# Kernel tuning notes

Hardware: AMD Instinct MI355X
Metric: run time of the kernel (lower is better)

## Reference

```python
import jax, jax.numpy as jnp
import numpy as np

B, N = 2, 6
H, W = 64, 64            # BEV grid
FH, FW = 32, 88          # camera feature map
DIM, FEAT_DIM = 128, 128
HEADS, DH = 4, 32
QW1, QW2 = 8, 8          # query window
KW1, KW2 = 4, 11         # key/val window
IMG_H, IMG_W = 224, 480
EPS = 1e-5


def _ln(t, g, b):
    m = t.mean(-1, keepdims=True)
    v = ((t - m) ** 2).mean(-1, keepdims=True)
    return (t - m) / jnp.sqrt(v + EPS) * g + b


def _bn_relu_conv(t, g, b, Wc):
    # eval-mode BatchNorm2d (running_mean=0, running_var=1) -> ReLU -> 1x1 conv
    y = jax.nn.relu(t / jnp.sqrt(1.0 + EPS) * g[:, None, None] + b[:, None, None])
    return jnp.einsum('oc,nchw->nohw', Wc, y)


def _normalize(t, axis):
    n = jnp.sqrt(jnp.sum(t * t, axis=axis, keepdims=True))
    return t / jnp.maximum(n, 1e-12)


def _win(t, w1, w2):
    # (..., X*w1, Y*w2, d) -> (..., X, Y, w1, w2, d)
    s = t.shape
    t = t.reshape(*s[:-3], s[-3] // w1, w1, s[-2] // w2, w2, s[-1])
    return jnp.swapaxes(t, -4, -3)


def _unwin(t):
    # (..., X, Y, w1, w2, d) -> (..., X*w1, Y*w2, d)
    s = t.shape
    return jnp.swapaxes(t, -4, -3).reshape(*s[:-5], s[-5] * s[-3], s[-4] * s[-2], s[-1])


def _gridwin(t, w1, w2):
    bb, nn, Ht, Wt, d = t.shape
    t = t.reshape(bb, nn, w1, Ht // w1, w2, Wt // w2, d)
    return t.transpose(0, 1, 3, 5, 2, 4, 6)  # (b, n, X, Y, w1, w2, d)


def _cross_win_attn(qw, kw, vw, ln_g, ln_b, Wqkv, bqkv, Wp, bp, skip):
    b, n, X, Y, w1, w2, d = qw.shape
    f1, f2 = kw.shape[4], kw.shape[5]
    L = X * Y
    q = qw.transpose(0, 2, 3, 1, 4, 5, 6).reshape(b, L, n * w1 * w2, d)
    k = kw.transpose(0, 2, 3, 1, 4, 5, 6).reshape(b, L, n * f1 * f2, d)
    v = vw.transpose(0, 2, 3, 1, 4, 5, 6).reshape(b, L, n * f1 * f2, d)
    q = _ln(q, ln_g[0], ln_b[0]) @ Wqkv[0] + bqkv[0]
    k = _ln(k, ln_g[1], ln_b[1]) @ Wqkv[1] + bqkv[1]
    v = _ln(v, ln_g[2], ln_b[2]) @ Wqkv[2] + bqkv[2]
    split = lambda t: t.reshape(*t.shape[:-1], HEADS, DH)  # head-major channel split
    q, k, v = split(q), split(k), split(v)
    att = jax.nn.softmax(DH ** -0.5 * jnp.einsum('blqhd,blkhd->bhlqk', q, k), axis=-1)
    o = jnp.einsum('bhlqk,blkhd->blqhd', att, v).reshape(b, L, n * w1 * w2, HEADS * DH)
    o = o @ Wp + bp
    o = o.reshape(b, X, Y, n, w1, w2, d).mean(3)  # mean over cameras
    return o + skip


def _forward(x, grid, feature, I_inv, E_inv,
             bn_fl_g, bn_fl_b, W_fl, bn_fp_g, bn_fp_b, W_fp,
             W_bev, b_bev, W_img, W_cam,
             attn_ln_g, attn_ln_b, attn_Wqkv, attn_bqkv, attn_Wp, attn_bp,
             pn_g, pn_b, Wma, bma, Wmb, bmb, post_g, post_b):
    b, n = feature.shape[:2]
    # image plane (buffer)
    xs = jnp.linspace(0.0, 1.0, FW) * IMG_W
    ys = jnp.linspace(0.0, 1.0, FH) * IMG_H
    gx, gy = jnp.meshgrid(xs, ys)  # (FH, FW) each
    plane = jnp.stack([gx, gy, jnp.ones_like(gx)], 0).reshape(3, FH * FW)
    # camera embedding from translation column of E_inv
    c = E_inv[..., -1]                                   # (b, n, 4)
    c_embed = jnp.einsum('oc,bnc->bno', W_cam, c)        # (b, n, dim)
    # unprojected rays
    cam = jnp.einsum('bnij,jk->bnik', I_inv, plane)      # (b, n, 3, HW)
    cam = jnp.concatenate([cam, jnp.ones_like(cam[:, :, :1])], 2)
    d = jnp.einsum('bnij,bnjk->bnik', E_inv, cam)        # (b, n, 4, HW)
    d_img = d.reshape(b, n, 4, FH, FW)
    d_embed = jnp.einsum('oc,bnchw->bnohw', W_img, d_img)
    img_embed = _normalize(d_embed - c_embed[..., None, None], axis=2)
    # BEV positional embedding
    w_embed = jnp.einsum('oc,chw->ohw', W_bev, grid[:2]) + b_bev[:, None, None]
    bev_embed = _normalize(w_embed[None, None] - c_embed[..., None, None], axis=2)  # (b,n,dim,H,W)
    feat = feature.reshape(b * n, FEAT_DIM, FH, FW)
    key_im = img_embed + _bn_relu_conv(feat, bn_fp_g, bn_fp_b, W_fp).reshape(b, n, DIM, FH, FW)
    val_im = _bn_relu_conv(feat, bn_fl_g, bn_fl_b, W_fl).reshape(b, n, DIM, FH, FW)
    query = bev_embed + x[:, None]                       # (b, n, dim, H, W)
    # channel-last
    q_im = query.transpose(0, 1, 3, 4, 2)
    k_im = key_im.transpose(0, 1, 3, 4, 2)
    v_im = val_im.transpose(0, 1, 3, 4, 2)
    x_im = x.transpose(0, 2, 3, 1)
    # stage 1: local windows
    qw = _win(q_im, QW1, QW2)
    kw = _win(k_im, KW1, KW2)
    vw = _win(v_im, KW1, KW2)
    o1 = _cross_win_attn(qw, kw, vw, attn_ln_g[0], attn_ln_b[0], attn_Wqkv[0],
                         attn_bqkv[0], attn_Wp[0], attn_bp[0], _win(x_im, QW1, QW2))
    q1 = _unwin(o1)                                      # (b, H, W, d)
    q1 = q1 + jax.nn.gelu(_ln(q1, pn_g[0], pn_b[0]) @ Wma[0] + bma[0], approximate=False) @ Wmb[0] + bmb[0]
    # stage 2: grid (swapped) windows
    qg = jnp.broadcast_to(q1[:, None], (b, n) + q1.shape[1:])
    o2 = _cross_win_attn(_win(qg, QW1, QW2), _gridwin(k_im, KW1, KW2), _gridwin(v_im, KW1, KW2),
                         attn_ln_g[1], attn_ln_b[1], attn_Wqkv[1], attn_bqkv[1],
                         attn_Wp[1], attn_bp[1], _win(q1, QW1, QW2))
    q2 = _unwin(o2)
    q2 = q2 + jax.nn.gelu(_ln(q2, pn_g[1], pn_b[1]) @ Wma[1] + bma[1], approximate=False) @ Wmb[1] + bmb[1]
    out = _ln(q2, post_g, post_b)
    return out.transpose(0, 3, 1, 2)                     # (b, dim, H, W)


def setup_inputs() -> dict:
    key = jax.random.key(0)
    ks = jax.random.split(key, 16)
    rn = lambda i, shape, sc=0.02: jax.random.normal(ks[i], shape, dtype=jnp.float32) * sc
    return {
        'index': 0,
        'x': jax.random.normal(ks[0], (B, DIM, H, W), dtype=jnp.float32),
        'grid': jax.random.normal(ks[1], (2, H, W), dtype=jnp.float32),
        'feature': jax.random.normal(ks[2], (B, N, FEAT_DIM, FH, FW), dtype=jnp.float32),
        'I_inv': jax.random.normal(ks[3], (B, N, 3, 3), dtype=jnp.float32),
        'E_inv': jax.random.normal(ks[4], (B, N, 4, 4), dtype=jnp.float32),
        'bn_fl_g': jnp.ones((FEAT_DIM,), jnp.float32), 'bn_fl_b': jnp.zeros((FEAT_DIM,), jnp.float32),
        'W_fl': rn(5, (DIM, FEAT_DIM)),
        'bn_fp_g': jnp.ones((FEAT_DIM,), jnp.float32), 'bn_fp_b': jnp.zeros((FEAT_DIM,), jnp.float32),
        'W_fp': rn(6, (DIM, FEAT_DIM)),
        'W_bev': rn(7, (DIM, 2)), 'b_bev': jnp.zeros((DIM,), jnp.float32),
        'W_img': rn(8, (DIM, 4)), 'W_cam': rn(9, (DIM, 4)),
        'attn_ln_g': jnp.ones((2, 3, DIM), jnp.float32), 'attn_ln_b': jnp.zeros((2, 3, DIM), jnp.float32),
        'attn_Wqkv': rn(10, (2, 3, DIM, HEADS * DH)), 'attn_bqkv': jnp.zeros((2, 3, HEADS * DH), jnp.float32),
        'attn_Wp': rn(11, (2, HEADS * DH, DIM)), 'attn_bp': jnp.zeros((2, DIM), jnp.float32),
        'pn_g': jnp.ones((2, DIM), jnp.float32), 'pn_b': jnp.zeros((2, DIM), jnp.float32),
        'Wma': rn(12, (2, DIM, 2 * DIM)), 'bma': jnp.zeros((2, 2 * DIM), jnp.float32),
        'Wmb': rn(13, (2, 2 * DIM, DIM)), 'bmb': jnp.zeros((2, DIM), jnp.float32),
        'post_g': jnp.ones((DIM,), jnp.float32), 'post_b': jnp.zeros((DIM,), jnp.float32),
    }


def reference(index, x, grid, feature, I_inv, E_inv,
              bn_fl_g, bn_fl_b, W_fl, bn_fp_g, bn_fp_b, W_fp,
              W_bev, b_bev, W_img, W_cam,
              attn_ln_g, attn_ln_b, attn_Wqkv, attn_bqkv, attn_Wp, attn_bp,
              pn_g, pn_b, Wma, bma, Wmb, bmb, post_g, post_b):
    del index  # grid for this index is passed directly
    return _forward(x, grid, feature, I_inv, E_inv,
                    bn_fl_g, bn_fl_b, W_fl, bn_fp_g, bn_fp_b, W_fp,
                    W_bev, b_bev, W_img, W_cam,
                    attn_ln_g, attn_ln_b, attn_Wqkv, attn_bqkv, attn_Wp, attn_bp,
                    pn_g, pn_b, Wma, bma, Wmb, bmb, post_g, post_b)
```

## Files before the change

kernel.cpp:

```cpp
#include <hip/hip_runtime.h>
#include <math.h>


typedef __attribute__((ext_vector_type(8))) short short8;
typedef __attribute__((ext_vector_type(4))) float f32x4;

__device__ __forceinline__ unsigned short f2bf(float f){
  union { float f; unsigned u; } v; v.f = f;
  unsigned r = v.u + 0x7FFF + ((v.u >> 16) & 1);
  return (unsigned short)(r >> 16);
}
__device__ __forceinline__ float bf2f(unsigned short h){
  union { unsigned u; float f; } v; v.u = ((unsigned)h) << 16; return v.f;
}
__device__ __forceinline__ void store_bf16x8(unsigned short* p, const float* v){
  union { short8 s8; unsigned short u[8]; } u;
  #pragma unroll
  for (int i=0;i<8;i++) u.u[i] = f2bf(v[i]);
  *(short8*)p = u.s8;
}

__device__ __forceinline__ float gelu_erf(float x){
  float z = x * 0.70710678118654752f;
  float a = fabsf(z);
// ... 151 lines not shown
      float sq = 0.f;
      #pragma unroll 8
      for (int k=0;k<64;k++){
        int c = half*64 + k;
        float4 w = sWI4[c];
        float de = w.x*d0 + w.y*d1 + w.z*d2 + w.w*d3 - sCE[c];
        sA[r*KP_ + c] = f2bf(de);
        sq = fmaf(de, de, sq);
      }
      sq += __shfl_xor(sq, 1);
      if (half == 0) sRn[r] = 1.0f / fmaxf(sqrtf(sq), 1e-12f);
    }
    {
      const float* Wsrc = qkv + m1*16384;
      const float* gvv = lg + m1*128;
      for (int idx = tid; idx < 8192; idx += 256){
        int n = idx & 127, k2 = (idx >> 7) << 1;
        float v0 = Wsrc[(size_t)k2*128 + n]     * gvv[k2];
        float v1 = Wsrc[(size_t)(k2+1)*128 + n] * gvv[k2+1];
        *(unsigned*)&sW[n*KP_ + k2] = (unsigned)f2bf(v0) | ((unsigned)f2bf(v1) << 16);
      }
    }
    __syncthreads();
    #pragma unroll
    for (int mt=0; mt<8; mt++){
      #pragma unroll
      for (int nt=0; nt<2; nt++){
        int col = n0 + nt*16 + lane15;
        #pragma unroll
        for (int r4=0; r4<4; r4++){
          int row = mt*16 + quad*4 + r4;
          float v = acc[mt][nt][r4];
          if (!which) v += bf2f(sA[row*KP_ + col]) * sRn[row];
          sA[row*KP_ + col] = f2bf(v);
        }
      }
    }
    __syncthreads();
    {
      int r = tid >> 1, part = tid & 1;
      float s=0.f, s2=0.f;
      #pragma unroll 8
      for (int k=0;k<64;k++){
        float v = bf2f(sA[r*KP_ + part*64 + k]);
        s += v; s2 = fmaf(v,v,s2);
      }
      s += __shfl_xor(s, 1); s2 += __shfl_xor(s2, 1);
      if (part == 0){
        float mean = s*(1.f/128.f);
        sMean[r] = mean;
        sRstd[r] = rsqrtf(fmaxf(s2*(1.f/128.f) - mean*mean, 0.f) + 1e-5f);
      }
    }
    __syncthreads();
    for (int i = tid; i < 2048; i += 256){
      int row = i >> 4, seg = i & 15;
      float mean = sMean[row], rstd = sRstd[row];
      union { short8 s; unsigned short u[8]; } t;
      t.s = *(const short8*)&sA[row*KP_ + seg*8];
      float v[8];
      #pragma unroll
      for (int k=0;k<8;k++) v[k] = (bf2f(t.u[k]) - mean)*rstd;
      store_bf16x8(&sA[row*KP_ + seg*8], v);
    }
    __syncthreads();
    #pragma unroll
    for (int mt=0; mt<8; mt++){ acc[mt][0]=(f32x4)0.f; acc[mt][1]=(f32x4)0.f; }
    #pragma unroll
    for (int kk=0; kk<4; kk++){
      short8 af[8], bf2v[2];
      #pragma unroll
      for (int mt=0; mt<8; mt++) af[mt] = *(const short8*)(aptr + mt*16*KP_ + kk*32);
      bf2v[0] = *(const short8*)(bptr + kk*32);
      bf2v[1] = *(const short8*)(bptr + 16*KP_ + kk*32);
      #pragma unroll
      for (int mt=0; mt<8; mt++){
        acc[mt][0] = __builtin_amdgcn_mfma_f32_16x16x32_bf16(af[mt], bf2v[0], acc[mt][0], 0,0,0);
        acc[mt][1] = __builtin_amdgcn_mfma_f32_16x16x32_bf16(af[mt], bf2v[1], acc[mt][1], 0,0,0);
      }
    }
    __syncthreads();
    #pragma unroll
    for (int mt=0; mt<8; mt++){
      #pragma unroll
      for (int nt=0; nt<2; nt++){
        int col = n0 + nt*16 + lane15;
        float bsv = sB1[col];
        #pragma unroll
        for (int r4=0; r4<4; r4++){
          int row = mt*16 + quad*4 + r4;
          sW[row*KP_ + col] = f2bf(acc[mt][nt][r4] + bsv);
        }
      }
    }
    __syncthreads();
    for (int i = tid; i < 2048; i += 256){
      int row = i >> 4, seg = i & 15;
      size_t orow = remap_kv(base + row, 1);
      *(short8*)(Oa + orow*128 + seg*8) = *(const short8*)&sW[row*KP_ + seg*8];
    }
    __syncthreads();
    {
      const float* Wsrc = qkv + m2*16384;
      const float* gvv = lg + m2*128;
      for (int idx = tid; idx < 8192; idx += 256){
        int n = idx & 127, k2 = (idx >> 7) << 1;
        float v0 = Wsrc[(size_t)k2*128 + n]     * gvv[k2];
        float v1 = Wsrc[(size_t)(k2+1)*128 + n] * gvv[k2+1];
        *(unsigned*)&sW[n*KP_ + k2] = (unsigned)f2bf(v0) | ((unsigned)f2bf(v1) << 16);
      }
    }
    __syncthreads();
    #pragma unroll
    for (int mt=0; mt<8; mt++){ acc[mt][0]=(f32x4)0.f; acc[mt][1]=(f32x4)0.f; }
    #pragma unroll
    for (int kk=0; kk<4; kk++){
      short8 af[8], bf2v[2];
      #pragma unroll
      for (int mt=0; mt<8; mt++) af[mt] = *(const short8*)(aptr + mt*16*KP_ + kk*32);
      bf2v[0] = *(const short8*)(bptr + kk*32);
      bf2v[1] = *(const short8*)(bptr + 16*KP_ + kk*32);
      #pragma unroll
      for (int mt=0; mt<8; mt++){
        acc[mt][0] = __builtin_amdgcn_mfma_f32_16x16x32_bf16(af[mt], bf2v[0], acc[mt][0], 0,0,0);
        acc[mt][1] = __builtin_amdgcn_mfma_f32_16x16x32_bf16(af[mt], bf2v[1], acc[mt][1], 0,0,0);
      }
    }
    __syncthreads();
    #pragma unroll
    for (int mt=0; mt<8; mt++){
      #pragma unroll
      for (int nt=0; nt<2; nt++){
        int col = n0 + nt*16 + lane15;
        float bsv = sB2[col];
        #pragma unroll
        for (int r4=0; r4<4; r4++){
          int row = mt*16 + quad*4 + r4;
          sA[row*KP_ + col] = f2bf(acc[mt][nt][r4] + bsv);
        }
      }
    }
    __syncthreads();
    for (int i = tid; i < 2048; i += 256){
      int row = i >> 4, seg = i & 15;
      size_t orow = remap_kv(base + row, 2);
      *(short8*)(Ob + orow*128 + seg*8) = *(const short8*)&sA[row*KP_ + seg*8];
    }
  } else if (bid < 1040){
    const float QSCALE = 0.17677669529663687f;
    float* sx = sMisc;
    int* rowoff = (int*)(sMisc + 2176);
    int bid2 = bid - 528;
    int b = bid2 >> 8; int pp0 = (bid2 & 255) << 4;
    for (int idx = tid; idx < 16384; idx += 256){
      int n = idx & 127, k = idx >> 7;
      sW[n*KP_ + k] = f2bf(qkv[(size_t)k*128 + n]);
    }
    {
      int cg = tid >> 4, px = tid & 15;
      #pragma unroll
      for (int i=0;i<8;i++){
        int c = cg + 16*i;
        sx[c*17 + px] = x[(size_t)b*524288 + (size_t)c*4096 + pp0 + px];
      }
    }
    if (tid < 16){
      int pix = pp0 + tid; int h = pix >> 6, w = pix & 63;
      int l = (h>>3)*8 + (w>>3); int tq = (h&7)*8 + (w&7);
      rowoff[tid] = (b*64 + l)*384 + tq;
    }
    __syncthreads();
    int xid = tid >> 4, part = tid & 15;
    int pix = pp0 + xid;
    float g0 = gridp[pix], g1 = gridp[4096 + pix];
    float we[8], xv[8];
    #pragma unroll
    for (int k=0;k<8;k++){
      int o = part*8 + k;
      we[k] = Wbev[o*2]*g0 + Wbev[o*2+1]*g1 + bbev[o];
      xv[k] = sx[(part*8+k)*17 + xid];
    }
    for (int n=0; n<6; n++){
      const float* E = Einv + (b*6+n)*16;
      float v[8]; float sq = 0.f;
      #pragma unroll
      for (int k=0;k<8;k++){
        int o = part*8 + k;
        const float* Wc = Wcam + o*4;
        float ce = Wc[0]*E[3] + Wc[1]*E[7] + Wc[2]*E[11] + Wc[3]*E[15];
        float vv = we[k] - ce;
        v[k] = vv; sq = fmaf(vv, vv, sq);
      }
      #pragma unroll
      for (int off=8; off>0; off>>=1) sq += __shfl_xor(sq, off, 16);
      float rn = 1.0f / fmaxf(sqrtf(sq), 1e-12f);
      float q[8]; float s=0.f, s2=0.f;
      #pragma unroll
      for (int k=0;k<8;k++){
        q[k] = fmaf(v[k], rn, xv[k]);
        s += q[k]; s2 = fmaf(q[k], q[k], s2);
      }
      #pragma unroll
      for (int off=8; off>0; off>>=1){ s += __shfl_xor(s, off, 16); s2 += __shfl_xor(s2, off, 16); }
      float mean = s*(1.f/128.f);
      float rstd = rsqrtf(fmaxf(s2*(1.f/128.f) - mean*mean, 0.f) + 1e-5f);
      float o8[8];
      #pragma unroll
      for (int k=0;k<8;k++){
        int c = part*8 + k;
        o8[k] = fmaf((q[k]-mean)*rstd, lg[c], lb[c]);
      }
      store_bf16x8(sA + (size_t)(n*16 + xid)*KP_ + part*8, o8);
    }
    __syncthreads();
    const int lane = tid & 63, wv = tid >> 6;
    const int lane15 = lane & 15, quad = lane >> 4;
    const int n0 = wv * 32;
    f32x4 acc[6][2];
    #pragma unroll
    for (int mt=0; mt<6; mt++){ acc[mt][0]=(f32x4)0.f; acc[mt][1]=(f32x4)0.f; }
    const unsigned short* aptr = sA + lane15*KP_ + quad*8;
    const unsigned short* bptr = sW + (size_t)(n0 + lane15)*KP_ + quad*8;
    #pragma unroll
    for (int kk=0; kk<4; kk++){
      short8 af[6], bf2v[2];
      #pragma unroll
      for (int mt=0; mt<6; mt++) af[mt] = *(const short8*)(aptr + mt*16*KP_ + kk*32);
      bf2v[0] = *(const short8*)(bptr + kk*32);
      bf2v[1] = *(const short8*)(bptr + 16*KP_ + kk*32);
      #pragma unroll
      for (int mt=0; mt<6; mt++){
        acc[mt][0] = __builtin_amdgcn_mfma_f32_16x16x32_bf16(af[mt], bf2v[0], acc[mt][0], 0,0,0);
        acc[mt][1] = __builtin_amdgcn_mfma_f32_16x16x32_bf16(af[mt], bf2v[1], acc[mt][1], 0,0,0);
      }
    }
    __syncthreads();
    #pragma unroll
    for (int nt=0; nt<2; nt++){
      int col = n0 + nt*16 + lane15;
      float bsv = abqkv[col];
      #pragma unroll
      for (int mt=0; mt<6; mt++){
        #pragma unroll
        for (int r4=0; r4<4; r4++){
          int row = mt*16 + quad*4 + r4;
          sA[row*KP_ + col] = f2bf((acc[mt][nt][r4] + bsv) * QSCALE);
        }
      }
    }
    __syncthreads();
    for (int i = tid; i < 1536; i += 256){
      int r = i >> 4, seg = i & 15;
      size_t grow = (size_t)rowoff[r & 15] + (r >> 4)*64;
      *(short8*)(QPh + grow*128 + seg*8) = *(const short8*)&sA[r*KP_ + seg*8];
    }
  } else if (bid < 1076){
    const int sel[9]  = {0, 1,1, 2,2, 3,3,3,3};
    const int soff[9] = {49152, 0,16384, 0,32768, 0,16384,32768,49152};
    const int doff[9] = {49152, 98304,114688, 131072,163840,
                         196608,212992,229376,245760};
    const int Ns[9]   = {128, 128,128, 256,256, 128,128,128,128};
    int bidw = bid - 1040;
    int sg = bidw >> 2, q = bidw & 3;
    const float* srcs[4] = {qkv, wp, wma, wmb};
    const float* src = srcs[sel[sg]] + soff[sg];
    unsigned short* dst = Wt + doff[sg];
    int K = 128, N = Ns[sg];
    int quarter = (K*N) >> 2;
    bool fold = (sg == 0);
    const float* gv = lg + 384;
    for (int idx = q*quarter + tid; idx < (q+1)*quarter; idx += 256){
      int n = idx / K, k = idx - n*K;
      float v = src[k*N + n];
      if (fold) v *= gv[k];
      dst[idx] = f2bf(v);
    }
  } else {
    if (tid < 128){
      int n = tid;
      const float* lnb = lb + 384;
      const float* W = qkv + 49152;
      float s = abqkv[384 + n];
      for (int k=0;k<128;k++) s = fmaf(lnb[k], W[k*128 + n], s);
      biasP[384 + n] = s;
    }
  }
}

__global__ __launch_bounds__(256) void k_tail(
    const unsigned short* __restrict__ AOh,
    const float* __restrict__ skipf, int skipmode,
    const unsigned short* __restrict__ WtP, const float* __restrict__ abp,
    const float* __restrict__ png, const float* __restrict__ pnb,
    const unsigned short* __restrict__ WtMAa, const unsigned short* __restrict__ WtMAb,
    const float* __restrict__ bma,
    const unsigned short* __restrict__ WtMBa, const unsigned short* __restrict__ WtMBb,
    const float* __restrict__ bmb,
    float* __restrict__ Q1out,
    const unsigned short* __restrict__ WtQ2, const float* __restrict__ q2bias,
    float q2scale, unsigned short* __restrict__ QPout,
    const float* __restrict__ postg, const float* __restrict__ postb,
    float* __restrict__ out){
  constexpr int KP_ = 136;
  __shared__ unsigned short sW[128*KP_];
  __shared__ unsigned short sX[32*KP_];
  __shared__ unsigned short sH1[32*KP_];
  __shared__ unsigned short sH2[32*KP_];
  __shared__ float sCUR[32*132];
  __shared__ float sbias[128];
  __shared__ float sg[128], sb2[128];
  __shared__ float sMean[32], sRstd[32];
  const int tid = threadIdx.x;
  const int base = blockIdx.x * 32;
  const int lane = tid & 63, wv = tid >> 6;
  const int lane15 = lane & 15, quad = lane >> 4;
  const int n0 = wv * 32;

  auto loadW = [&](const unsigned short* Wp){
    for (int i = tid; i < 2048; i += 256){
      int n = i >> 4, k8 = (i & 15) << 3;
      *(short8*)&sW[n*KP_ + k8] = *(const short8*)(Wp + (size_t)n*128 + k8);
    }
  };
  auto domfma = [&](const unsigned short* Asrc, f32x4 acc[2][2]){
    const unsigned short* aptr = Asrc + lane15*KP_ + quad*8;
    const unsigned short* bptr = sW + (size_t)(n0 + lane15)*KP_ + quad*8;
    #pragma unroll
    for (int kk=0; kk<4; kk++){
      short8 a0 = *(const short8*)(aptr + kk*32);
      short8 a1 = *(const short8*)(aptr + 16*KP_ + kk*32);
      short8 b0 = *(const short8*)(bptr + kk*32);
      short8 b1 = *(const short8*)(bptr + 16*KP_ + kk*32);
      acc[0][0] = __builtin_amdgcn_mfma_f32_16x16x32_bf16(a0,b0,acc[0][0],0,0,0);
      acc[1][0] = __builtin_amdgcn_mfma_f32_16x16x32_bf16(a1,b0,acc[1][0],0,0,0);
      acc[0][1] = __builtin_amdgcn_mfma_f32_16x16x32_bf16(a0,b1,acc[0][1],0,0,0);
      acc[1][1] = __builtin_amdgcn_mfma_f32_16x16x32_bf16(a1,b1,acc[1][1],0,0,0);
    }
  };

  loadW(WtP);
  {
    const int r = tid >> 3, part = tid & 7;
    const short8* src = (const short8*)(AOh + (size_t)(base+r)*128 + part*16);
    short8* dst = (short8*)(sX + r*KP_ + part*16);
    dst[0] = src[0]; dst[1] = src[1];
  }
  if (tid < 128){ sbias[tid] = abp[tid]; sg[tid] = png[tid]; sb2[tid] = pnb[tid]; }
  __syncthreads();
  {
    f32x4 acc[2][2];
    acc[0][0]=(f32x4)0.f; acc[0][1]=(f32x4)0.f;
    acc[1][0]=(f32x4)0.f; acc[1][1]=(f32x4)0.f;
    domfma(sX, acc);
    #pragma unroll
    for (int mt=0; mt<2; mt++)
      #pragma unroll
      for (int nt=0; nt<2; nt++){
        int col = n0 + nt*16 + lane15;
        float bsv = sbias[col];
        #pragma unroll
        for (int r4=0; r4<4; r4++){
          int row = mt*16 + quad*4 + r4;
          int rrow = base + row;
          float v = acc[mt][nt][r4] + bsv;
          if (skipmode == 1){
            int bb = rrow >> 12, l = (rrow >> 6) & 63, pp = rrow & 63;
            int pix = (((l>>3)*8 + (pp>>3)) << 6) + (l&7)*8 + (pp&7);
            v += skipf[(size_t)bb*524288 + (size_t)col*4096 + pix];
          } else {
            v += skipf[(size_t)rrow*128 + col];
          }
          sCUR[row*132 + col] = v;
        }
      }
  }
  __syncthreads();
  loadW(WtMAa);
  if (tid < 128) sbias[tid] = bma[tid];
  {
    const int r = tid >> 3, part = tid & 7;
    float v[16];
    #pragma unroll
    for (int k=0;k<16;k++) v[k] = sCUR[r*132 + part*16 + k];
    float s=0.f, s2=0.f;
    #pragma unroll
    for (int k=0;k<16;k++){ s += v[k]; s2 = fmaf(v[k],v[k],s2); }
    #pragma unroll
    for (int off=4; off>0; off>>=1){ s += __shfl_xor(s, off, 8); s2 += __shfl_xor(s2, off, 8); }
    float mean = s*(1.f/128.f);
    float rstd = rsqrtf(fmaxf(s2*(1.f/128.f) - mean*mean, 0.f) + 1e-5f);
    #pragma unroll
    for (int k=0;k<16;k++){
      int c = part*16 + k;
      v[k] = fmaf((v[k]-mean)*rstd, sg[c], sb2[c]);
    }
    store_bf16x8(sX + r*KP_ + part*16, v);
    store_bf16x8(sX + r*KP_ + part*16 + 8, v+8);
  }
  __syncthreads();
  {
    f32x4 acc[2][2];
    acc[0][0]=(f32x4)0.f; acc[0][1]=(f32x4)0.f;
    acc[1][0]=(f32x4)0.f; acc[1][1]=(f32x4)0.f;
    domfma(sX, acc);
    #pragma unroll
    for (int mt=0; mt<2; mt++)
      #pragma unroll
      for (int nt=0; nt<2; nt++){
        int col = n0 + nt*16 + lane15;
        float bsv = sbias[col];
        #pragma unroll
        for (int r4=0; r4<4; r4++){
          int row = mt*16 + quad*4 + r4;
          sH1[row*KP_ + col] = f2bf(gelu_erf(acc[mt][nt][r4] + bsv));
        }
      }
  }
  __syncthreads();
  loadW(WtMAb);
  if (tid < 128) sbias[tid] = bma[128 + tid];
  __syncthreads();
  {
    f32x4 acc[2][2];
    acc[0][0]=(f32x4)0.f; acc[0][1]=(f32x4)0.f;
    acc[1][0]=(f32x4)0.f; acc[1][1]=(f32x4)0.f;
    domfma(sX, acc);
    #pragma unroll
    for (int mt=0; mt<2; mt++)
      #pragma unroll
      for (int nt=0; nt<2; nt++){
        int col = n0 + nt*16 + lane15;
        float bsv = sbias[col];
        #pragma unroll
        for (int r4=0; r4<4; r4++){
          int row = mt*16 + quad*4 + r4;
          sH2[row*KP_ + col] = f2bf(gelu_erf(acc[mt][nt][r4] + bsv));
        }
      }
  }
  __syncthreads();
  loadW(WtMBa);
  if (tid < 128) sbias[tid] = bmb[tid];
  __syncthreads();
  f32x4 acc[2][2];
  acc[0][0]=(f32x4)0.f; acc[0][1]=(f32x4)0.f;
  acc[1][0]=(f32x4)0.f; acc[1][1]=(f32x4)0.f;
  domfma(sH1, acc);
  __syncthreads();
  loadW(WtMBb);
  __syncthreads();
  domfma(sH2, acc);
  if (out == nullptr){
    #pragma unroll
    for (int mt=0; mt<2; mt++)
      #pragma unroll
      for (int nt=0; nt<2; nt++){
        int col = n0 + nt*16 + lane15;
        float bsv = sbias[col];
        #pragma unroll
        for (int r4=0; r4<4; r4++){
          int row = mt*16 + quad*4 + r4;
          float v = acc[mt][nt][r4] + bsv + sCUR[row*132 + col];
          sCUR[row*132 + col] = v;
          Q1out[(size_t)(base+row)*128 + col] = v;
        }
      }
    __syncthreads();
    {
      const int r = tid >> 3, part = tid & 7;
      float s=0.f, s2=0.f;
      #pragma unroll
      for (int k=0;k<16;k++){
        float v = sCUR[r*132 + part*16 + k];
        s += v; s2 = fmaf(v,v,s2);
      }
      #pragma unroll
      for (int off=4; off>0; off>>=1){ s += __shfl_xor(s, off, 8); s2 += __shfl_xor(s2, off, 8); }
      if (part == 0){
        float mean = s*(1.f/128.f);
        sMean[r] = mean;
        sRstd[r] = rsqrtf(fmaxf(s2*(1.f/128.f) - mean*mean, 0.f) + 1e-5f);
      }
    }
    __syncthreads();
    {
      const int r = tid >> 3, part = tid & 7;
      float mean = sMean[r], rstd = sRstd[r];
      float v[16];
      #pragma unroll
      for (int k=0;k<16;k++) v[k] = (sCUR[r*132 + part*16 + k] - mean)*rstd;
      store_bf16x8(sX + r*KP_ + part*16, v);
      store_bf16x8(sX + r*KP_ + part*16 + 8, v+8);
    }
    loadW(WtQ2);
    if (tid < 128) sbias[tid] = q2bias[tid];
    __syncthreads();
    f32x4 a2[2][2];
    a2[0][0]=(f32x4)0.f; a2[0][1]=(f32x4)0.f;
    a2[1][0]=(f32x4)0.f; a2[1][1]=(f32x4)0.f;
    domfma(sX, a2);
    #pragma unroll
    for (int mt=0; mt<2; mt++)
      #pragma unroll
      for (int nt=0; nt<2; nt++){
        int col = n0 + nt*16 + lane15;
        float bsv = sbias[col];
        #pragma unroll
        for (int r4=0; r4<4; r4++){
          int row = mt*16 + quad*4 + r4;
          sH1[row*KP_ + col] = f2bf((a2[mt][nt][r4] + bsv) * q2scale);
        }
      }
    __syncthreads();
    for (int i = tid; i < 512; i += 256){
      int row = i >> 4, seg = i & 15;
      *(short8*)(QPout + (size_t)(base+row)*128 + seg*8) = *(const short8*)&sH1[row*KP_ + seg*8];
    }
  } else {
    float res[2][2][4];
    #pragma unroll
    for (int mt=0; mt<2; mt++)
      #pragma unroll
      for (int nt=0; nt<2; nt++){
        int col = n0 + nt*16 + lane15;
        float bsv = sbias[col];
        #pragma unroll
        for (int r4=0; r4<4; r4++){
          int row = mt*16 + quad*4 + r4;
          res[mt][nt][r4] = acc[mt][nt][r4] + bsv + sCUR[row*132 + col];
        }
      }
    __syncthreads();
    #pragma unroll
    for (int mt=0; mt<2; mt++)
      #pragma unroll
      for (int nt=0; nt<2; nt++){
        int col = n0 + nt*16 + lane15;
        #pragma unroll
        for (int r4=0; r4<4; r4++){
          int row = mt*16 + quad*4 + r4;
          sCUR[row*132 + col] = res[mt][nt][r4];
        }
      }
    __syncthreads();
    {
      const int r = tid >> 3, part = tid & 7;
      float s=0.f, s2=0.f;
      #pragma unroll
      for (int k=0;k<16;k++){
        float v = sCUR[r*132 + part*16 + k];
        s += v; s2 = fmaf(v,v,s2);
      }
      #pragma unroll
      for (int off=4; off>0; off>>=1){ s += __shfl_xor(s, off, 8); s2 += __shfl_xor(s2, off, 8); }
      if (part == 0){
        float mean = s*(1.f/128.f);
        sMean[r] = mean;
        sRstd[r] = rsqrtf(fmaxf(s2*(1.f/128.f) - mean*mean, 0.f) + 1e-5f);
      }
    }
    __syncthreads();
    {
      int c = tid & 127, half = tid >> 7;
      int b = base >> 12, l = (base >> 6) & 63, p0 = base & 63;
      float go = postg[c], bo = postb[c];
      #pragma unroll
      for (int seg=0; seg<2; seg++){
        int p = p0 + half*16 + seg*8;
        int hrow = (l>>3)*8 + (p>>3);
        int w0 = (l&7)*8;
        float rr[8];
        #pragma unroll
        for (int j=0;j<8;j++){
          int row = half*16 + seg*8 + j;
          rr[j] = fmaf((sCUR[row*132 + c] - sMean[row])*sRstd[row], go, bo);
        }
        size_t obase = ((size_t)(b*128 + c))*4096 + (size_t)hrow*64 + w0;
        *(float4*)&out[obase]   = make_float4(rr[0],rr[1],rr[2],rr[3]);
        *(float4*)&out[obase+4] = make_float4(rr[4],rr[5],rr[6],rr[7]);
      }
    }
  }
}

__global__ __launch_bounds__(256) void k_attn2(const unsigned short* __restrict__ QPh,
    const unsigned short* __restrict__ KPh, const unsigned short* __restrict__ VPh,
    unsigned short* __restrict__ AOh, int nrep, int nQ){
  __shared__ unsigned short Ksh[288*40];
  __shared__ unsigned short Vt[32*296];
  __shared__ unsigned short Psh[4*16*40];
  __shared__ float rs[4*16];
  int hd = blockIdx.x & 3; int bl = blockIdx.x >> 2;
  size_t kvbase = (size_t)bl*264;
  int tid = threadIdx.x;
  for (int idx = tid; idx < 1056; idx += 256){
    int row = idx >> 2, seg = idx & 3;
    *(short8*)&Ksh[row*40 + seg*8] =
      *(const short8*)(KPh + (kvbase+row)*128 + hd*32 + seg*8);
  }
  for (int idx = tid; idx < 96; idx += 256){
    int row = 264 + (idx>>2), seg = idx & 3;
    short8 z = {0,0,0,0,0,0,0,0};
    *(short8*)&Ksh[row*40 + seg*8] = z;
  }
  for (int idx = tid; idx < 528; idx += 256){
    int kp = idx >> 2, seg = idx & 3;
    union { short8 s; unsigned short u[8]; } a, b;
    a.s = *(const short8*)(VPh + (kvbase + 2*kp)*128 + hd*32 + seg*8);
    b.s = *(const short8*)(VPh + (kvbase + 2*kp + 1)*128 + hd*32 + seg*8);
    #pragma unroll
    for (int i=0;i<8;i++)
      *(unsigned*)&Vt[(seg*8+i)*296 + 2*kp] = (unsigned)a.u[i] | ((unsigned)b.u[i] << 16);
  }
  for (int idx = tid; idx < 384; idx += 256){
    int d = idx / 12, kp = 264 + (idx % 12)*2;
    *(unsigned*)&Vt[d*296 + kp] = 0u;
  }
  __syncthreads();
  const int wv = tid >> 6, lane = tid & 63;
  const int lane15 = lane & 15, quad = lane >> 4;
  unsigned short* Pw = Psh + wv*640;
  float* rsw = rs + wv*16;
  short8 vfrag[9][2];
  #pragma unroll
  for (int kc=0; kc<9; kc++){
    vfrag[kc][0] = *(const short8*)&Vt[(lane15)*296      + kc*32 + quad*8];
    vfrag[kc][1] = *(const short8*)&Vt[(16+lane15)*296   + kc*32 + quad*8];
  }
  f32x4 macc0 = (f32x4)0.f, macc1 = (f32x4)0.f;
  for (int cam = 0; cam < nrep; cam++){
    int qrow = bl*nQ + (cam*4 + wv)*16 + lane15;
    short8 qf = *(const short8*)(QPh + (size_t)qrow*128 + hd*32 + quad*8);
    f32x4 oa0 = (f32x4)0.f, oa1 = (f32x4)0.f;
    float rsum = 0.f;
    #pragma unroll
    for (int kc=0; kc<9; kc++){
      #pragma unroll
      for (int sub=0; sub<2; sub++){
        int kt = kc*2 + sub;
        short8 kf = *(const short8*)&Ksh[(kt*16 + lane15)*40 + quad*8];
        f32x4 st = __builtin_amdgcn_mfma_f32_16x16x32_bf16(kf, qf, (f32x4)0.f, 0,0,0);
        int kbase = kt*16 + quad*4;
        float e0 = (kbase+0 < 264) ? __expf(st[0]) : 0.f;
        float e1 = (kbase+1 < 264) ? __expf(st[1]) : 0.f;
        float e2 = (kbase+2 < 264) ? __expf(st[2]) : 0.f;
        float e3 = (kbase+3 < 264) ? __expf(st[3]) : 0.f;
        rsum += (e0+e1)+(e2+e3);
        uint2 pk;
        pk.x = (unsigned)f2bf(e0) | ((unsigned)f2bf(e1) << 16);
        pk.y = (unsigned)f2bf(e2) | ((unsigned)f2bf(e3) << 16);
        *(uint2*)&Pw[lane15*40 + sub*16 + quad*4] = pk;
      }
      short8 pf = *(const short8*)&Pw[lane15*40 + quad*8];
      oa0 = __builtin_amdgcn_mfma_f32_16x16x32_bf16(pf, vfrag[kc][0], oa0, 0,0,0);
      oa1 = __builtin_amdgcn_mfma_f32_16x16x32_bf16(pf, vfrag[kc][1], oa1, 0,0,0);
    }
    rsum += __shfl_xor(rsum, 16);
    rsum += __shfl_xor(rsum, 32);
    if (lane < 16) rsw[lane] = rsum;
    f32x4 rv = *(f32x4*)&rsw[quad*4];
    #pragma unroll
    for (int r=0;r<4;r++){
      float inv = 1.f / rv[r];
      macc0[r] = fmaf(oa0[r], inv, macc0[r]);
      macc1[r] = fmaf(oa1[r], inv, macc1[r]);
    }
  }
  float sc = (nrep == 6) ? (1.f/6.f) : 1.f;
  int pixb = wv*16 + quad*4;
  #pragma unroll
  for (int r=0;r<4;r++){
    size_t rowo = ((size_t)(bl*64 + pixb + r))*128 + hd*32;
    AOh[rowo + lane15]      = f2bf(macc0[r]*sc);
    AOh[rowo + 16 + lane15] = f2bf(macc1[r]*sc);
  }
}

extern "C" void kernel_launch(void* const* d_in, const int* in_sizes, int n_in,
                              void* d_out, int out_size, void* d_ws, size_t ws_size,
                              hipStream_t stream) {
  (void)in_sizes; (void)n_in; (void)out_size; (void)ws_size;
  const float* x     = (const float*)d_in[1];
  const float* gridp = (const float*)d_in[2];
  const float* feat  = (const float*)d_in[3];
  const float* Iinv  = (const float*)d_in[4];
  const float* Einv  = (const float*)d_in[5];
  const float* gfl   = (const float*)d_in[6];
  const float* bfl   = (const float*)d_in[7];
  const float* Wfl   = (const float*)d_in[8];
  const float* gfp   = (const float*)d_in[9];
  const float* bfp   = (const float*)d_in[10];
  const float* Wfp   = (const float*)d_in[11];
  const float* Wbev  = (const float*)d_in[12];
  const float* bbev  = (const float*)d_in[13];
  const float* Wimg  = (const float*)d_in[14];
  const float* Wcam  = (const float*)d_in[15];
  const float* alng  = (const float*)d_in[16];
  const float* alnb  = (const float*)d_in[17];
  const float* aWqkv = (const float*)d_in[18];
  const float* abqkv = (const float*)d_in[19];
  const float* aWp   = (const float*)d_in[20];
  const float* abp   = (const float*)d_in[21];
  const float* png   = (const float*)d_in[22];
  const float* pnb   = (const float*)d_in[23];
  const float* Wma   = (const float*)d_in[24];
  const float* bma   = (const float*)d_in[25];
  const float* Wmb   = (const float*)d_in[26];
  const float* bmb   = (const float*)d_in[27];
  const float* postg = (const float*)d_in[28];
  const float* postb = (const float*)d_in[29];
  float* out = (float*)d_out;
  float* ws  = (float*)d_ws;
  const float QSC = 0.17677669529663687f;

  float* biasP = ws;
  unsigned short* Wt   = (unsigned short*)(ws + 2048);
  unsigned short* K1h  = (unsigned short*)(ws + 149504);
  unsigned short* V1h  = K1h + 4325376;
  unsigned short* KPh  = V1h + 4325376;
  unsigned short* VPh  = KPh + 4325376;
  unsigned short* KP2h = VPh + 4325376;
  unsigned short* VP2h = KP2h + 4325376;
  unsigned short* QPh  = VP2h + 4325376;
  unsigned short* Qbh  = QPh + 6291456;
  unsigned short* AOh  = Qbh + 6291456;
  float* Q1f = (float*)(AOh + 1048576);

  unsigned short* WtQ2 = Wt + 49152;
  unsigned short* WtP1 = Wt + 98304;    unsigned short* WtP2 = Wt + 114688;
  unsigned short* WtMA1 = Wt + 131072;  unsigned short* WtMA2 = Wt + 163840;
  unsigned short* WtMB1a = Wt + 196608; unsigned short* WtMB1b = Wt + 212992;
  unsigned short* WtMB2a = Wt + 229376; unsigned short* WtMB2b = Wt + 245760;

  k_prepconv<<<1077, 256, 0, stream>>>(aWqkv, aWp, Wma, Wmb, Wt,
      abqkv, biasP, gridp, Wbev, bbev, x, alng, alnb, Einv, Wcam, QPh,
      feat, gfp, bfp, Wfp, gfl, bfl, Wfl, Iinv, Wimg,
      KPh, KP2h, VPh, VP2h);

  k_attn2<<<512, 256, 0, stream>>>(QPh, KPh, VPh, AOh, 6, 384);
  k_tail<<<256, 256, 0, stream>>>(AOh, x, 1, WtP1, abp, png, pnb,
      WtMA1, WtMA1+16384, bma, WtMB1a, WtMB1b, bmb, Q1f,
      WtQ2, biasP+384, QSC, QPh,
      nullptr, nullptr, nullptr);
  k_attn2<<<512, 256, 0, stream>>>(QPh, KP2h, VP2h, AOh, 1, 64);
  k_tail<<<256, 256, 0, stream>>>(AOh, Q1f, 3, WtP2, abp+128, png+128, pnb+128,
      WtMA2, WtMA2+16384, bma+256, WtMB2a, WtMB2b, bmb+128, nullptr,
      nullptr, nullptr, 0.f, nullptr,
      postg, postb, out);
}
```

Baseline: 252.5 us.

## Fuse window attention into tail MLP kernel, dropping AO round-trip

Merges the attention kernel and the projection/MLP tail into one kernel per stage. Each block now computes attention for 32 query rows across all 4 heads (two passes of 2 heads) and writes the result straight into shared memory for the tail GEMMs, so the bf16 attention output no longer goes through global memory and two launches are removed. In exchange the grid shrinks from 512 to 256 blocks and shared memory grows to about 82 KB through a union buffer, which lowers occupancy. Each block also reloads K/V for its window, so the two blocks sharing a window both fetch it. The stage-2 Q is written to a separate buffer, Qbh.

New measurement: 274.4 us. +8.7%, slower.

```diff
diff --git a/kernel.cpp b/kernel.cpp
--- a/kernel.cpp
+++ b/kernel.cpp
@@ -462,8 +462,10 @@
   }
 }
 
-__global__ __launch_bounds__(256) void k_tail(
-    const unsigned short* __restrict__ AOh,
+__global__ __launch_bounds__(256) void k_fused(
+    const unsigned short* __restrict__ Qsrc,
+    const unsigned short* __restrict__ Ksrc, const unsigned short* __restrict__ Vsrc,
+    int nrep, int nQ,
     const float* __restrict__ skipf, int skipmode,
     const unsigned short* __restrict__ WtP, const float* __restrict__ abp,
     const float* __restrict__ png, const float* __restrict__ pnb,
@@ -477,20 +479,120 @@
     const float* __restrict__ postg, const float* __restrict__ postb,
     float* __restrict__ out){
   constexpr int KP_ = 136;
-  __shared__ unsigned short sW[128*KP_];
-  __shared__ unsigned short sX[32*KP_];
-  __shared__ unsigned short sH1[32*KP_];
-  __shared__ unsigned short sH2[32*KP_];
-  __shared__ float sCUR[32*132];
-  __shared__ float sbias[128];
-  __shared__ float sg[128], sb2[128];
-  __shared__ float sMean[32], sRstd[32];
+  __shared__ __align__(16) unsigned char U[82432];
+  unsigned short* Ksh = (unsigned short*)U;
+  unsigned short* Vt  = (unsigned short*)(U + 39168);
+  unsigned short* Psh = (unsigned short*)(U + 77056);
+  float* rs           = (float*)(U + 82176);
+  unsigned short* sW  = (unsigned short*)U;
+  unsigned short* sX  = (unsigned short*)(U + 34816);
+  unsigned short* sH1 = (unsigned short*)(U + 43520);
+  unsigned short* sH2 = (unsigned short*)(U + 52224);
+  float* sCUR  = (float*)(U + 60928);
+  float* sbias = (float*)(U + 77824);
+  float* sg    = (float*)(U + 78336);
+  float* sb2   = (float*)(U + 78848);
+  float* sMean = (float*)(U + 79360);
+  float* sRstd = (float*)(U + 79488);
   const int tid = threadIdx.x;
-  const int base = blockIdx.x * 32;
   const int lane = tid & 63, wv = tid >> 6;
   const int lane15 = lane & 15, quad = lane >> 4;
+  const int bl = blockIdx.x >> 1, half = blockIdx.x & 1;
+  const int base = blockIdx.x * 32;
+  const int hl = wv >> 1, qh = wv & 1;
+  size_t kvbase = (size_t)bl*264;
+  float resv[2][2][4];
+
+  #pragma unroll
+  for (int p = 0; p < 2; p++){
+    for (int idx = tid; idx < 2112; idx += 256){
+      int row = idx >> 3, seg = idx & 7;
+      *(short8*)&Ksh[row*68 + seg*8] =
+        *(const short8*)(Ksrc + (kvbase+row)*128 + p*64 + seg*8);
+    }
+    for (int idx = tid; idx < 192; idx += 256){
+      int row = 264 + (idx>>3), seg = idx & 7;
+      short8 z = {0,0,0,0,0,0,0,0};
+      *(short8*)&Ksh[row*68 + seg*8] = z;
+    }
+    for (int idx = tid; idx < 1056; idx += 256){
+      int kp = idx >> 3, seg = idx & 7;
+      union { short8 s; unsigned short u[8]; } a, b;
+      a.s = *(const short8*)(Vsrc + (kvbase + 2*kp)*128 + p*64 + seg*8);
+      b.s = *(const short8*)(Vsrc + (kvbase + 2*kp + 1)*128 + p*64 + seg*8);
+      #pragma unroll
+      for (int i=0;i<8;i++)
+        *(unsigned*)&Vt[(seg*8+i)*296 + 2*kp] = (unsigned)a.u[i] | ((unsigned)b.u[i] << 16);
+    }
+    for (int idx = tid; idx < 768; idx += 256){
+      int d = idx / 12, kp = 132 + (idx - (idx/12)*12);
+      *(unsigned*)&Vt[d*296 + 2*kp] = 0u;
+    }
+    __syncthreads();
+    unsigned short* Pw = Psh + wv*640;
+    float* rsw = rs + wv*16;
+    short8 vfrag[9][2];
+    #pragma unroll
+    for (int kc=0; kc<9; kc++){
+      vfrag[kc][0] = *(const short8*)&Vt[(hl*32 + lane15)*296      + kc*32 + quad*8];
+      vfrag[kc][1] = *(const short8*)&Vt[(hl*32 + 16 + lane15)*296 + kc*32 + quad*8];
+    }
+    f32x4 macc0 = (f32x4)0.f, macc1 = (f32x4)0.f;
+    for (int cam = 0; cam < nrep; cam++){
+      int qrow = bl*nQ + cam*64 + half*32 + qh*16 + lane15;
+      short8 qf = *(const short8*)(Qsrc + (size_t)qrow*128 + p*64 + hl*32 + quad*8);
+      f32x4 oa0 = (f32x4)0.f, oa1 = (f32x4)0.f;
+      float rsum = 0.f;
+      #pragma unroll
+      for (int kc=0; kc<9; kc++){
+        #pragma unroll
+        for (int sub=0; sub<2; sub++){
+          int kt = kc*2 + sub;
+          short8 kf = *(const short8*)&Ksh[(kt*16 + lane15)*68 + hl*32 + quad*8];
+          f32x4 st = __builtin_amdgcn_mfma_f32_16x16x32_bf16(kf, qf, (f32x4)0.f, 0,0,0);
+          int kb = kt*16 + quad*4;
+          float e0 = (kb+0 < 264) ? __expf(st[0]) : 0.f;
+          float e1 = (kb+1 < 264) ? __expf(st[1]) : 0.f;
+          float e2 = (kb+2 < 264) ? __expf(st[2]) : 0.f;
+          float e3 = (kb+3 < 264) ? __expf(st[3]) : 0.f;
+          rsum += (e0+e1)+(e2+e3);
+          uint2 pk;
+          pk.x = (unsigned)f2bf(e0) | ((unsigned)f2bf(e1) << 16);
+          pk.y = (unsigned)f2bf(e2) | ((unsigned)f2bf(e3) << 16);
+          *(uint2*)&Pw[lane15*40 + sub*16 + quad*4] = pk;
+        }
+        short8 pf = *(const short8*)&Pw[lane15*40 + quad*8];
+        oa0 = __builtin_amdgcn_mfma_f32_16x16x32_bf16(pf, vfrag[kc][0], oa0, 0,0,0);
+        oa1 = __builtin_amdgcn_mfma_f32_16x16x32_bf16(pf, vfrag[kc][1], oa1, 0,0,0);
+      }
+      rsum += __shfl_xor(rsum, 16);
+      rsum += __shfl_xor(rsum, 32);
+      if (lane < 16) rsw[lane] = rsum;
+      f32x4 rv = *(f32x4*)&rsw[quad*4];
+      #pragma unroll
+      for (int r=0;r<4;r++){
+        float inv = 1.f / rv[r];
+        macc0[r] = fmaf(oa0[r], inv, macc0[r]);
+        macc1[r] = fmaf(oa1[r], inv, macc1[r]);
+      }
+    }
+    float sc = (nrep == 6) ? (1.f/6.f) : 1.f;
+    #pragma unroll
+    for (int r=0;r<4;r++){ resv[p][0][r]=macc0[r]*sc; resv[p][1][r]=macc1[r]*sc; }
+    __syncthreads();
+  }
+  #pragma unroll
+  for (int p=0;p<2;p++)
+    #pragma unroll
+    for (int nt=0;nt<2;nt++)
+      #pragma unroll
+      for (int r=0;r<4;r++){
+        int row = qh*16 + quad*4 + r;
+        int col = p*64 + hl*32 + nt*16 + lane15;
+        sX[row*KP_ + col] = f2bf(resv[p][nt][r]);
+      }
+
   const int n0 = wv * 32;
-
   auto loadW = [&](const unsigned short* Wp){
     for (int i = tid; i < 2048; i += 256){
       int n = i >> 4, k8 = (i & 15) << 3;
@@ -514,12 +616,6 @@
   };
 
   loadW(WtP);
-  {
-    const int r = tid >> 3, part = tid & 7;
-    const short8* src = (const short8*)(AOh + (size_t)(base+r)*128 + part*16);
-    short8* dst = (short8*)(sX + r*KP_ + part*16);
-    dst[0] = src[0]; dst[1] = src[1];
-  }
   if (tid < 128){ sbias[tid] = abp[tid]; sg[tid] = png[tid]; sb2[tid] = pnb[tid]; }
   __syncthreads();
   {
@@ -736,18 +832,18 @@
     }
     __syncthreads();
     {
-      int c = tid & 127, half = tid >> 7;
+      int c = tid & 127, hf = tid >> 7;
       int b = base >> 12, l = (base >> 6) & 63, p0 = base & 63;
       float go = postg[c], bo = postb[c];
       #pragma unroll
       for (int seg=0; seg<2; seg++){
-        int p = p0 + half*16 + seg*8;
+        int p = p0 + hf*16 + seg*8;
         int hrow = (l>>3)*8 + (p>>3);
         int w0 = (l&7)*8;
         float rr[8];
         #pragma unroll
         for (int j=0;j<8;j++){
-          int row = half*16 + seg*8 + j;
+          int row = hf*16 + seg*8 + j;
           rr[j] = fmaf((sCUR[row*132 + c] - sMean[row])*sRstd[row], go, bo);
         }
         size_t obase = ((size_t)(b*128 + c))*4096 + (size_t)hrow*64 + w0;
@@ -755,99 +851,6 @@
         *(float4*)&out[obase+4] = make_float4(rr[4],rr[5],rr[6],rr[7]);
       }
     }
-  }
-}
-
-__global__ __launch_bounds__(256) void k_attn2(const unsigned short* __restrict__ QPh,
-    const unsigned short* __restrict__ KPh, const unsigned short* __restrict__ VPh,
-    unsigned short* __restrict__ AOh, int nrep, int nQ){
-  __shared__ unsigned short Ksh[288*40];
-  __shared__ unsigned short Vt[32*296];
-  __shared__ unsigned short Psh[4*16*40];
-  __shared__ float rs[4*16];
-  int hd = blockIdx.x & 3; int bl = blockIdx.x >> 2;
-  size_t kvbase = (size_t)bl*264;
-  int tid = threadIdx.x;
-  for (int idx = tid; idx < 1056; idx += 256){
-    int row = idx >> 2, seg = idx & 3;
-    *(short8*)&Ksh[row*40 + seg*8] =
-      *(const short8*)(KPh + (kvbase+row)*128 + hd*32 + seg*8);
-  }
-  for (int idx = tid; idx < 96; idx += 256){
-    int row = 264 + (idx>>2), seg = idx & 3;
-    short8 z = {0,0,0,0,0,0,0,0};
-    *(short8*)&Ksh[row*40 + seg*8] = z;
-  }
-  for (int idx = tid; idx < 528; idx += 256){
-    int kp = idx >> 2, seg = idx & 3;
-    union { short8 s; unsigned short u[8]; } a, b;
-    a.s = *(const short8*)(VPh + (kvbase + 2*kp)*128 + hd*32 + seg*8);
-    b.s = *(const short8*)(VPh + (kvbase + 2*kp + 1)*128 + hd*32 + seg*8);
-    #pragma unroll
-    for (int i=0;i<8;i++)
-      *(unsigned*)&Vt[(seg*8+i)*296 + 2*kp] = (unsigned)a.u[i] | ((unsigned)b.u[i] << 16);
-  }
-  for (int idx = tid; idx < 384; idx += 256){
-    int d = idx / 12, kp = 264 + (idx % 12)*2;
-    *(unsigned*)&Vt[d*296 + kp] = 0u;
-  }
-  __syncthreads();
-  const int wv = tid >> 6, lane = tid & 63;
-  const int lane15 = lane & 15, quad = lane >> 4;
-  unsigned short* Pw = Psh + wv*640;
-  float* rsw = rs + wv*16;
-  short8 vfrag[9][2];
-  #pragma unroll
-  for (int kc=0; kc<9; kc++){
-    vfrag[kc][0] = *(const short8*)&Vt[(lane15)*296      + kc*32 + quad*8];
-    vfrag[kc][1] = *(const short8*)&Vt[(16+lane15)*296   + kc*32 + quad*8];
-  }
-  f32x4 macc0 = (f32x4)0.f, macc1 = (f32x4)0.f;
-  for (int cam = 0; cam < nrep; cam++){
-    int qrow = bl*nQ + (cam*4 + wv)*16 + lane15;
-    short8 qf = *(const short8*)(QPh + (size_t)qrow*128 + hd*32 + quad*8);
-    f32x4 oa0 = (f32x4)0.f, oa1 = (f32x4)0.f;
-    float rsum = 0.f;
-    #pragma unroll
-    for (int kc=0; kc<9; kc++){
-      #pragma unroll
-      for (int sub=0; sub<2; sub++){
-        int kt = kc*2 + sub;
-        short8 kf = *(const short8*)&Ksh[(kt*16 + lane15)*40 + quad*8];
-        f32x4 st = __builtin_amdgcn_mfma_f32_16x16x32_bf16(kf, qf, (f32x4)0.f, 0,0,0);
-        int kbase = kt*16 + quad*4;
-        float e0 = (kbase+0 < 264) ? __expf(st[0]) : 0.f;
-        float e1 = (kbase+1 < 264) ? __expf(st[1]) : 0.f;
-        float e2 = (kbase+2 < 264) ? __expf(st[2]) : 0.f;
-        float e3 = (kbase+3 < 264) ? __expf(st[3]) : 0.f;
-        rsum += (e0+e1)+(e2+e3);
-        uint2 pk;
-        pk.x = (unsigned)f2bf(e0) | ((unsigned)f2bf(e1) << 16);
-        pk.y = (unsigned)f2bf(e2) | ((unsigned)f2bf(e3) << 16);
-        *(uint2*)&Pw[lane15*40 + sub*16 + quad*4] = pk;
-      }
-      short8 pf = *(const short8*)&Pw[lane15*40 + quad*8];
-      oa0 = __builtin_amdgcn_mfma_f32_16x16x32_bf16(pf, vfrag[kc][0], oa0, 0,0,0);
-      oa1 = __builtin_amdgcn_mfma_f32_16x16x32_bf16(pf, vfrag[kc][1], oa1, 0,0,0);
-    }
-    rsum += __shfl_xor(rsum, 16);
-    rsum += __shfl_xor(rsum, 32);
-    if (lane < 16) rsw[lane] = rsum;
-    f32x4 rv = *(f32x4*)&rsw[quad*4];
-    #pragma unroll
-    for (int r=0;r<4;r++){
-      float inv = 1.f / rv[r];
-      macc0[r] = fmaf(oa0[r], inv, macc0[r]);
-      macc1[r] = fmaf(oa1[r], inv, macc1[r]);
-    }
-  }
-  float sc = (nrep == 6) ? (1.f/6.f) : 1.f;
-  int pixb = wv*16 + quad*4;
-  #pragma unroll
-  for (int r=0;r<4;r++){
-    size_t rowo = ((size_t)(bl*64 + pixb + r))*128 + hd*32;
-    AOh[rowo + lane15]      = f2bf(macc0[r]*sc);
-    AOh[rowo + 16 + lane15] = f2bf(macc1[r]*sc);
   }
 }
 
@@ -912,14 +915,13 @@
       feat, gfp, bfp, Wfp, gfl, bfl, Wfl, Iinv, Wimg,
       KPh, KP2h, VPh, VP2h);
 
-  k_attn2<<<512, 256, 0, stream>>>(QPh, KPh, VPh, AOh, 6, 384);
-  k_tail<<<256, 256, 0, stream>>>(AOh, x, 1, WtP1, abp, png, pnb,
-      WtMA1, WtMA1+16384, bma, WtMB1a, WtMB1b, bmb, Q1f,
-      WtQ2, biasP+384, QSC, QPh,
+  k_fused<<<256, 256, 0, stream>>>(QPh, KPh, VPh, 6, 384,
+      x, 1, WtP1, abp, png, pnb, WtMA1, WtMA1+16384, bma,
+      WtMB1a, WtMB1b, bmb, Q1f, WtQ2, biasP+384, QSC, Qbh,
       nullptr, nullptr, nullptr);
-  k_attn2<<<512, 256, 0, stream>>>(QPh, KP2h, VP2h, AOh, 1, 64);
-  k_tail<<<256, 256, 0, stream>>>(AOh, Q1f, 3, WtP2, abp+128, png+128, pnb+128,
-      WtMA2, WtMA2+16384, bma+256, WtMB2a, WtMB2b, bmb+128, nullptr,
-      nullptr, nullptr, 0.f, nullptr,
+
+  k_fused<<<256, 256, 0, stream>>>(Qbh, KP2h, VP2h, 1, 64,
+      Q1f, 3, WtP2, abp+128, png+128, pnb+128, WtMA2, WtMA2+16384, bma+256,
+      WtMB2a, WtMB2b, bmb+128, nullptr, nullptr, nullptr, 0.f, nullptr,
       postg, postb, out);
 }
```

## Prefetch next weight tile into registers during MFMA phases; pack qkv transpose stores

Applied to the files above, without the earlier changes.

The MLP kernel now loads each next 128x128 bf16 weight matrix from global memory into registers before the current MFMA phase, and writes it to shared memory after the barrier. This hides global load latency behind compute instead of stalling on each weight load. A separate change packs two bf16 values per 32-bit shared store in the qkv weight transpose loop, halving the store count. The register staging adds 8 short8 registers per thread, which raises register pressure and may reduce occupancy.

Result: faster. 240.9 us (-4.6%).

```diff
diff --git a/kernel.cpp b/kernel.cpp
--- a/kernel.cpp
+++ b/kernel.cpp
@@ -327,9 +327,11 @@
     int* rowoff = (int*)(sMisc + 2176);
     int bid2 = bid - 528;
     int b = bid2 >> 8; int pp0 = (bid2 & 255) << 4;
-    for (int idx = tid; idx < 16384; idx += 256){
-      int n = idx & 127, k = idx >> 7;
-      sW[n*KP_ + k] = f2bf(qkv[(size_t)k*128 + n]);
+    for (int idx = tid; idx < 8192; idx += 256){
+      int n = idx & 127, k2 = (idx >> 7) << 1;
+      float v0 = qkv[(size_t)k2*128 + n];
+      float v1 = qkv[(size_t)(k2+1)*128 + n];
+      *(unsigned*)&sW[n*KP_ + k2] = (unsigned)f2bf(v0) | ((unsigned)f2bf(v1) << 16);
     }
     {
       int cg = tid >> 4, px = tid & 15;
@@ -491,10 +493,21 @@
   const int lane15 = lane & 15, quad = lane >> 4;
   const int n0 = wv * 32;
 
-  auto loadW = [&](const unsigned short* Wp){
-    for (int i = tid; i < 2048; i += 256){
-      int n = i >> 4, k8 = (i & 15) << 3;
-      *(short8*)&sW[n*KP_ + k8] = *(const short8*)(Wp + (size_t)n*128 + k8);
+  short8 wreg[8];
+  auto stageLoad = [&](const unsigned short* Wp){
+    #pragma unroll
+    for (int i=0;i<8;i++){
+      int idx = tid + i*256;
+      int n = idx >> 4, k8 = (idx & 15) << 3;
+      wreg[i] = *(const short8*)(Wp + (size_t)n*128 + k8);
+    }
+  };
+  auto stageWrite = [&](){
+    #pragma unroll
+    for (int i=0;i<8;i++){
+      int idx = tid + i*256;
+      int n = idx >> 4, k8 = (idx & 15) << 3;
+      *(short8*)&sW[n*KP_ + k8] = wreg[i];
     }
   };
   auto domfma = [&](const unsigned short* Asrc, f32x4 acc[2][2]){
@@ -513,7 +526,7 @@
     }
   };
 
-  loadW(WtP);
+  stageLoad(WtP);
   {
     const int r = tid >> 3, part = tid & 7;
     const short8* src = (const short8*)(AOh + (size_t)(base+r)*128 + part*16);
@@ -521,7 +534,9 @@
     dst[0] = src[0]; dst[1] = src[1];
   }
   if (tid < 128){ sbias[tid] = abp[tid]; sg[tid] = png[tid]; sb2[tid] = pnb[tid]; }
+  stageWrite();
   __syncthreads();
+  stageLoad(WtMAa);
   {
     f32x4 acc[2][2];
     acc[0][0]=(f32x4)0.f; acc[0][1]=(f32x4)0.f;
@@ -550,7 +565,7 @@
       }
   }
   __syncthreads();
-  loadW(WtMAa);
+  stageWrite();
   if (tid < 128) sbias[tid] = bma[tid];
   {
     const int r = tid >> 3, part = tid & 7;
@@ -573,6 +588,7 @@
     store_bf16x8(sX + r*KP_ + part*16 + 8, v+8);
   }
   __syncthreads();
+  stageLoad(WtMAb);
   {
     f32x4 acc[2][2];
     acc[0][0]=(f32x4)0.f; acc[0][1]=(f32x4)0.f;
@@ -592,9 +608,10 @@
       }
   }
   __syncthreads();
-  loadW(WtMAb);
+  stageWrite();
   if (tid < 128) sbias[tid] = bma[128 + tid];
   __syncthreads();
+  stageLoad(WtMBa);
   {
     f32x4 acc[2][2];
     acc[0][0]=(f32x4)0.f; acc[0][1]=(f32x4)0.f;
@@ -614,16 +631,18 @@
       }
   }
   __syncthreads();
-  loadW(WtMBa);
+  stageWrite();
   if (tid < 128) sbias[tid] = bmb[tid];
   __syncthreads();
+  stageLoad(WtMBb);
   f32x4 acc[2][2];
   acc[0][0]=(f32x4)0.f; acc[0][1]=(f32x4)0.f;
   acc[1][0]=(f32x4)0.f; acc[1][1]=(f32x4)0.f;
   domfma(sH1, acc);
   __syncthreads();
-  loadW(WtMBb);
+  stageWrite();
   __syncthreads();
+  if (WtQ2) stageLoad(WtQ2);
   domfma(sH2, acc);
   if (out == nullptr){
     #pragma unroll
@@ -667,7 +686,7 @@
       store_bf16x8(sX + r*KP_ + part*16, v);
       store_bf16x8(sX + r*KP_ + part*16 + 8, v+8);
     }
-    loadW(WtQ2);
+    stageWrite();
     if (tid < 128) sbias[tid] = q2bias[tid];
     __syncthreads();
     f32x4 a2[2][2];
```
